# Optimization experiments

Measured on AMD Instinct MI355X. Metric: run time of the kernel, lower is better.

## Reference

```python
import jax, jax.numpy as jnp
import numpy as np


def setup_inputs() -> dict:
    key = jax.random.key(0)
    ks = jax.random.split(key, 6)
    N, E, D, L = 50000, 800000, 128, 2
    x = jax.random.normal(ks[0], (N, D), jnp.float32)
    h = jax.random.normal(ks[1], (L, N, D), jnp.float32)
    Wl = jax.random.normal(ks[2], (L, 6, D, D), jnp.float32) * 0.05  # neighbor (lin_l)
    Wr = jax.random.normal(ks[3], (L, 6, D, D), jnp.float32) * 0.05  # root (lin_r)
    b = jnp.zeros((L, 6, D), jnp.float32)
    src = jax.random.randint(ks[4], (E,), 0, N, jnp.int32)
    dst = jax.random.randint(ks[5], (E,), 0, N, jnp.int32)
    return {"x": x, "h": h, "Wl": Wl, "Wr": Wr, "b": b, "src": src, "dst": dst}


def reference(x, h, Wl, Wr, b, src, dst):
    # PyG SAGEConv (mean aggregation): out = mean_{j in N(i)} x_j @ W_l + x_i @ W_r + b
    N = x.shape[0]
    L = h.shape[0]
    deg = jax.ops.segment_sum(jnp.ones_like(src, jnp.float32), dst, num_segments=N)
    inv_deg = (1.0 / jnp.maximum(deg, 1.0))[:, None]  # [N,1]

    def sage(xin, l, g):
        agg = jax.ops.segment_sum(xin[src], dst, num_segments=N) * inv_deg  # [N,D]
        return agg @ Wl[l, g] + xin @ Wr[l, g] + b[l, g]

    outs = []
    inp = x
    for l in range(L):  # gates: 0=xz 1=hz 2=xr 3=hr 4=xh 5=hh
        z = jax.nn.sigmoid(sage(inp, l, 0) + sage(h[l], l, 1))
        r = jax.nn.sigmoid(sage(inp, l, 2) + sage(h[l], l, 3))
        h_tilde = jnp.tanh(sage(inp, l, 4) + sage(r * h[l], l, 5))
        out = z * h[l] + (1.0 - z) * h_tilde
        outs.append(out)
        inp = out
    return jnp.stack(outs)  # [L, N, D] == h_out
```

## Files before the change

kernel.cpp:

```cpp
#include <hip/hip_runtime.h>
#include <hip/hip_bf16.h>
#include <hip/hip_fp16.h>

#define D 128
#define BM 32
#define BN 128
#define LDSK 64
#define SCAN_BLK 1024

#define GLOBAL_AS __attribute__((address_space(1)))
#define LDS_AS __attribute__((address_space(3)))

typedef __attribute__((ext_vector_type(8))) __bf16 bf16x8;
typedef __attribute__((ext_vector_type(4))) float f32x4;
typedef __hip_bfloat16 bf16;

__device__ __forceinline__ float bf2f(bf16 v) { return __bfloat162float(v); }
__device__ __forceinline__ bf16 f2bf(float v) { return __float2bfloat16(v); }

__global__ void probe_kernel(const unsigned short* __restrict__ w, int n, int* __restrict__ flag) {
  __shared__ int cnt[256];
  int t = threadIdx.x;
  int bad = 0;
  int lim4 = n / 8 < 1024 ? n / 8 : 1024;
  const uint4* w4 = (const uint4*)w;
  for (int i = t; i < lim4; i += 256) {
    uint4 v = w4[i];
    unsigned int ws[8] = {v.x & 0xffffu, v.x >> 16, v.y & 0xffffu, v.y >> 16,
                          v.z & 0xffffu, v.z >> 16, v.w & 0xffffu, v.w >> 16};
#pragma unroll
    for (int j = 0; j < 8; ++j) {
      float f = __uint_as_float(ws[j] << 16);
      if (!(fabsf(f) <= 4.0f)) bad++;
    }
  }
  cnt[t] = bad;
  __syncthreads();
  for (int off = 128; off > 0; off >>= 1) {
    if (t < off) cnt[t] += cnt[t + off];
    __syncthreads();
  }
  if (t == 0) flag[0] = (cnt[0] > 512) ? 1 : 0;
}

__global__ void convert_kernel(const float* __restrict__ xf, const float* __restrict__ hf,
                               bf16* __restrict__ xb, bf16* __restrict__ hb,
                               const int* __restrict__ flag, int nx, int nh) {
  if (flag[0] == 0) return;
  int i = (blockIdx.x * blockDim.x + threadIdx.x) * 4;
  if (i + 3 < nx) {
    float4 v = *(const float4*)(xf + i);
    bf16 o[4] = {f2bf(v.x), f2bf(v.y), f2bf(v.z), f2bf(v.w)};
    *(ushort4*)(xb + i) = *(const ushort4*)o;
  } else {
    for (int j = 0; j < 4; ++j)
      if (i + j < nx) xb[i + j] = f2bf(xf[i + j]);
  }
  if (i + 3 < nh) {
    float4 v = *(const float4*)(hf + i);
    bf16 o[4] = {f2bf(v.x), f2bf(v.y), f2bf(v.z), f2bf(v.w)};
    *(ushort4*)(hb + i) = *(const ushort4*)o;
  } else {
    for (int j = 0; j < 4; ++j)
      if (i + j < nh) hb[i + j] = f2bf(hf[i + j]);
  }
}


__global__ void zero_int_kernel(int* p, int n) {
  int i = blockIdx.x * blockDim.x + threadIdx.x;
  if (i < n) p[i] = 0;
}

__global__ void count_deg_kernel(const int* __restrict__ dst, int* __restrict__ deg, int E) {
  int e = blockIdx.x * blockDim.x + threadIdx.x;
  if (e < E) atomicAdd(&deg[dst[e]], 1);
}

__global__ void scan1_kernel(const int* __restrict__ deg, int* __restrict__ bsum, int N) {
  __shared__ int lsum[256];
  int t = threadIdx.x;
  int base = blockIdx.x * SCAN_BLK + t * 4;
  int s = 0;
  if (base + 3 < N) {
    int4 v = *(const int4*)(deg + base);
    s = v.x + v.y + v.z + v.w;
  } else {
    for (int i = 0; i < 4; ++i)
      if (base + i < N) s += deg[base + i];
  }
  lsum[t] = s;
  __syncthreads();
  for (int off = 128; off > 0; off >>= 1) {
    if (t < off) lsum[t] += lsum[t + off];
    __syncthreads();
  }
  if (t == 0) bsum[blockIdx.x] = lsum[0];
}

__global__ void scan2_kernel(int* __restrict__ bsum, int nb) {
  __shared__ int sh[256];
  int t = threadIdx.x;
  sh[t] = (t < nb) ? bsum[t] : 0;
  __syncthreads();
  for (int off = 1; off < 256; off <<= 1) {
    int v = sh[t];
    int add = (t >= off) ? sh[t - off] : 0;
    __syncthreads();
    sh[t] = v + add;
    __syncthreads();
  }
  if (t < nb) bsum[t] = (t == 0) ? 0 : sh[t - 1];
}

__global__ void scan3_kernel(const int* __restrict__ deg, const int* __restrict__ bsum,
                             int* __restrict__ offs, int* __restrict__ cursor,
                             float* __restrict__ inv_deg, int N, int E) {
  __shared__ int lsum[256];
  int t = threadIdx.x;
  int base = blockIdx.x * SCAN_BLK + t * 4;
  int d0 = 0, d1 = 0, d2 = 0, d3 = 0;
  if (base + 3 < N) {
    int4 v = *(const int4*)(deg + base);
    d0 = v.x; d1 = v.y; d2 = v.z; d3 = v.w;
  } else {
    if (base + 0 < N) d0 = deg[base + 0];
    if (base + 1 < N) d1 = deg[base + 1];
    if (base + 2 < N) d2 = deg[base + 2];
    if (base + 3 < N) d3 = deg[base + 3];
  }
  lsum[t] = d0 + d1 + d2 + d3;
  __syncthreads();
  for (int off = 1; off < 256; off <<= 1) {
    int v = lsum[t];
    int add = (t >= off) ? lsum[t - off] : 0;
    __syncthreads();
    lsum[t] = v + add;
    __syncthreads();
  }
  int run = bsum[blockIdx.x] + ((t == 0) ? 0 : lsum[t - 1]);
  int dd[4] = {d0, d1, d2, d3};
  for (int i = 0; i < 4; ++i) {
    int idx = base + i;
    if (idx < N) {
      offs[idx] = run;
      cursor[idx] = run;
      inv_deg[idx] = 1.0f / (float)(dd[i] > 1 ? dd[i] : 1);
      run += dd[i];
    }
  }
  if (blockIdx.x == 0 && t == 0) offs[N] = E;
}

__global__ void scatter_kernel(const int* __restrict__ src, const int* __restrict__ dst,
                               int* __restrict__ cursor, int* __restrict__ esrc, int E) {
  int e = blockIdx.x * blockDim.x + threadIdx.x;
  if (e < E) {
    int pos = atomicAdd(&cursor[dst[e]], 1);
    esrc[pos] = src[e];
  }
}


__global__ void agg_kernel(const bf16* __restrict__ featA, const bf16* __restrict__ featB,
                           const int* __restrict__ flag, const int* __restrict__ esrc,
                           const int* __restrict__ offs, const float* __restrict__ inv_deg,
                           bf16* __restrict__ out, int N) {
  const bf16* feat = flag[0] ? featB : featA;
  int node = (int)((blockIdx.x * (size_t)blockDim.x + threadIdx.x) >> 6);
  int lane = threadIdx.x & 63;
  if (node >= N) return;
  int e0 = offs[node], e1 = offs[node + 1];
  float a0 = 0.f, a1 = 0.f;
  int c = lane * 2;
  for (int base = e0; base < e1; base += 64) {
    int cnt = e1 - base;
    if (cnt > 64) cnt = 64;
    int ei = base + lane;
    int idx = esrc[ei < e1 ? ei : (e1 - 1)];
    int j = 0;
    for (; j + 8 <= cnt; j += 8) {
      int s0 = __shfl(idx, j + 0, 64), s1 = __shfl(idx, j + 1, 64);
      int s2 = __shfl(idx, j + 2, 64), s3 = __shfl(idx, j + 3, 64);
      int s4 = __shfl(idx, j + 4, 64), s5 = __shfl(idx, j + 5, 64);
      int s6 = __shfl(idx, j + 6, 64), s7 = __shfl(idx, j + 7, 64);
      __hip_bfloat162 v0 = *(const __hip_bfloat162*)(feat + (size_t)s0 * D + c);
      __hip_bfloat162 v1 = *(const __hip_bfloat162*)(feat + (size_t)s1 * D + c);
      __hip_bfloat162 v2 = *(const __hip_bfloat162*)(feat + (size_t)s2 * D + c);
      __hip_bfloat162 v3 = *(const __hip_bfloat162*)(feat + (size_t)s3 * D + c);
      __hip_bfloat162 v4 = *(const __hip_bfloat162*)(feat + (size_t)s4 * D + c);
      __hip_bfloat162 v5 = *(const __hip_bfloat162*)(feat + (size_t)s5 * D + c);
      __hip_bfloat162 v6 = *(const __hip_bfloat162*)(feat + (size_t)s6 * D + c);
      __hip_bfloat162 v7 = *(const __hip_bfloat162*)(feat + (size_t)s7 * D + c);
      a0 += bf2f(v0.x) + bf2f(v1.x) + bf2f(v2.x) + bf2f(v3.x) +
            bf2f(v4.x) + bf2f(v5.x) + bf2f(v6.x) + bf2f(v7.x);
      a1 += bf2f(v0.y) + bf2f(v1.y) + bf2f(v2.y) + bf2f(v3.y) +
            bf2f(v4.y) + bf2f(v5.y) + bf2f(v6.y) + bf2f(v7.y);
    }
    for (; j < cnt; ++j) {
      int s = __shfl(idx, j, 64);
      __hip_bfloat162 v = *(const __hip_bfloat162*)(feat + (size_t)s * D + c);
      a0 += bf2f(v.x);
      a1 += bf2f(v.y);
    }
  }
  float w = inv_deg[node];
  __hip_bfloat162 o;
  o.x = f2bf(a0 * w);
  o.y = f2bf(a1 * w);
  *(__hip_bfloat162*)(out + (size_t)node * D + c) = o;
}

__global__ void agg_dual_kernel(const bf16* __restrict__ fAa, const bf16* __restrict__ fAb,
                                const bf16* __restrict__ fBa, const bf16* __restrict__ fBb,
                                const int* __restrict__ flag, const int* __restrict__ esrc,
                                const int* __restrict__ offs, const float* __restrict__ inv_deg,
                                bf16* __restrict__ outA, bf16* __restrict__ outB, int N) {
  int fl = flag[0];
  const bf16* fA = fl ? fAb : fAa;
  const bf16* fB = fl ? fBb : fBa;
  int node = (int)((blockIdx.x * (size_t)blockDim.x + threadIdx.x) >> 6);
  int lane = threadIdx.x & 63;
  if (node >= N) return;
  int e0 = offs[node], e1 = offs[node + 1];
  float a0 = 0.f, a1 = 0.f, b0 = 0.f, b1 = 0.f;
  int c = lane * 2;
  for (int base = e0; base < e1; base += 64) {
    int cnt = e1 - base;
    if (cnt > 64) cnt = 64;
    int ei = base + lane;
    int idx = esrc[ei < e1 ? ei : (e1 - 1)];
    int j = 0;
    for (; j + 4 <= cnt; j += 4) {
      int s0 = __shfl(idx, j + 0, 64), s1 = __shfl(idx, j + 1, 64);
      int s2 = __shfl(idx, j + 2, 64), s3 = __shfl(idx, j + 3, 64);
      size_t r0 = (size_t)s0 * D + c, r1 = (size_t)s1 * D + c;
      size_t r2 = (size_t)s2 * D + c, r3 = (size_t)s3 * D + c;
      __hip_bfloat162 va0 = *(const __hip_bfloat162*)(fA + r0);
      __hip_bfloat162 va1 = *(const __hip_bfloat162*)(fA + r1);
      __hip_bfloat162 va2 = *(const __hip_bfloat162*)(fA + r2);
      __hip_bfloat162 va3 = *(const __hip_bfloat162*)(fA + r3);
      __hip_bfloat162 vb0 = *(const __hip_bfloat162*)(fB + r0);
      __hip_bfloat162 vb1 = *(const __hip_bfloat162*)(fB + r1);
      __hip_bfloat162 vb2 = *(const __hip_bfloat162*)(fB + r2);
      __hip_bfloat162 vb3 = *(const __hip_bfloat162*)(fB + r3);
      a0 += bf2f(va0.x) + bf2f(va1.x) + bf2f(va2.x) + bf2f(va3.x);
      a1 += bf2f(va0.y) + bf2f(va1.y) + bf2f(va2.y) + bf2f(va3.y);
      b0 += bf2f(vb0.x) + bf2f(vb1.x) + bf2f(vb2.x) + bf2f(vb3.x);
      b1 += bf2f(vb0.y) + bf2f(vb1.y) + bf2f(vb2.y) + bf2f(vb3.y);
    }
    for (; j < cnt; ++j) {
      int s = __shfl(idx, j, 64);
      size_t ro = (size_t)s * D + c;
      __hip_bfloat162 va = *(const __hip_bfloat162*)(fA + ro);
      __hip_bfloat162 vb = *(const __hip_bfloat162*)(fB + ro);
      a0 += bf2f(va.x);
      a1 += bf2f(va.y);
      b0 += bf2f(vb.x);
      b1 += bf2f(vb.y);
    }
  }
  float w = inv_deg[node];
  __hip_bfloat162 oa, ob;
  oa.x = f2bf(a0 * w);
  oa.y = f2bf(a1 * w);
  ob.x = f2bf(b0 * w);
  ob.y = f2bf(b1 * w);
  *(__hip_bfloat162*)(outA + (size_t)node * D + c) = oa;
  *(__hip_bfloat162*)(outB + (size_t)node * D + c) = ob;
}


__device__ __forceinline__ float loadw(const void* p, size_t idx, int fl) {
  return fl ? ((const float*)p)[idx] : bf2f(((const bf16*)p)[idx]);
}

__global__ void pack_kernel(const void* __restrict__ Wl, const void* __restrict__ Wr,
                            const void* __restrict__ b, int l, const int* __restrict__ flag,
                            bf16* __restrict__ B1p, bf16* __restrict__ B2p,
                            float* __restrict__ bs1, float* __restrict__ bs2) {
  int fl = flag[0];
  int idx = blockIdx.x * blockDim.x + threadIdx.x;
  const int SZ1 = 256 * 512;
  const int SZ2 = 128 * 512;
  if (idx < SZ1) {
    int n = idx >> 9, k = idx & 511;
    int p = k >> 7, kr = k & 127;
    int gpair = n >> 7, nc = n & 127;
    int gate = gpair * 2 + (p >> 1);
    const void* W = (p & 1) ? Wr : Wl;
    B1p[idx] = f2bf(loadw(W, (((size_t)l * 6 + gate) * D + kr) * D + nc, fl));
  } else if (idx < SZ1 + SZ2) {
    int i2 = idx - SZ1;
    int n = i2 >> 9, k = i2 & 511;
    int p = k >> 7, kr = k & 127;
    int gate = 4 + (p >> 1);
    const void* W = (p & 1) ? Wr : Wl;
    B2p[i2] = f2bf(loadw(W, (((size_t)l * 6 + gate) * D + kr) * D + n, fl));
  } else if (idx < SZ1 + SZ2 + 384) {
    int c = idx - (SZ1 + SZ2);
    if (c < 256) {
      int g0 = (c >> 7) * 2;
      int cc = c & 127;
      bs1[c] = loadw(b, ((size_t)l * 6 + g0) * D + cc, fl) +
               loadw(b, ((size_t)l * 6 + g0 + 1) * D + cc, fl);
    } else {
      int cc = c - 256;
      bs2[cc] = loadw(b, ((size_t)l * 6 + 4) * D + cc, fl) +
                loadw(b, ((size_t)l * 6 + 5) * D + cc, fl);
    }
  }
}


__device__ __forceinline__ void stage_tile(const bf16* const (&Ablk)[4],
                                           const bf16* __restrict__ Bp, int M, int row0, int col0,
                                           bf16* As, bf16* Bs, int kt, int wave, int r_rel,
                                           int pslot) {
  const bf16* Aptr = Ablk[kt >> 1];
  const int kr = (kt & 1) * 64;
  {
    int rchunk = wave * 8;
    int r = rchunk + r_rel;
    int gsrc = pslot ^ (r & 7);
    int rg = row0 + r;
    if (rg > M - 1) rg = M - 1;
    const bf16* ga = Aptr + (size_t)rg * D + kr + gsrc * 8;
    bf16* la = As + rchunk * LDSK;
    __builtin_amdgcn_global_load_lds((const GLOBAL_AS unsigned int*)(const void*)ga,
                                     (LDS_AS unsigned int*)(void*)la, 16, 0, 0);
  }
#pragma unroll
  for (int i = 0; i < 4; ++i) {
    int rchunk = wave * 32 + i * 8;
    int r = rchunk + r_rel;
    int gsrc = pslot ^ (r & 7);
    const bf16* gb = Bp + (size_t)(col0 + r) * 512 + kt * 64 + gsrc * 8;
    bf16* lb = Bs + rchunk * LDSK;
    __builtin_amdgcn_global_load_lds((const GLOBAL_AS unsigned int*)(const void*)gb,
                                     (LDS_AS unsigned int*)(void*)lb, 16, 0, 0);
  }
}

__device__ __forceinline__ void gemm_mainloop(const bf16* A0, const bf16* A1, const bf16* A2,
                                              const bf16* A3, const bf16* __restrict__ Bp, int M,
                                              int row0, int col0, bf16* As, bf16* Bs,
                                              f32x4 (&acc)[1][4]) {
  int tid = threadIdx.x;
  int wave = tid >> 6, lane = tid & 63;
  int wrow = (wave >> 1) * 16, wcol = (wave & 1) * 64;
  const bf16* Ablk[4] = {A0, A1, A2, A3};
  int r_rel = lane >> 3;
  int pslot = lane & 7;
  int quad = lane >> 4, mr = lane & 15;
  const int ABUF = BM * LDSK;
  const int BBUF = BN * LDSK;

  stage_tile(Ablk, Bp, M, row0, col0, As, Bs, 0, wave, r_rel, pslot);
  __syncthreads();

#pragma unroll
  for (int kt = 0; kt < 8; ++kt) {
    const int cur = kt & 1;
    if (kt < 7)
      stage_tile(Ablk, Bp, M, row0, col0, As + (cur ^ 1) * ABUF, Bs + (cur ^ 1) * BBUF, kt + 1,
                 wave, r_rel, pslot);
    const bf16* Asc = As + cur * ABUF;
    const bf16* Bsc = Bs + cur * BBUF;
#pragma unroll
    for (int kk = 0; kk < 2; ++kk) {
      int G = kk * 4 + quad;
      bf16x8 af, bfv[4];
      {
        int R = wrow + mr;
        af = *(const bf16x8*)(const void*)(Asc + R * LDSK + ((G ^ (R & 7)) * 8));
      }
#pragma unroll
      for (int ni = 0; ni < 4; ++ni) {
        int R = wcol + ni * 16 + mr;
        bfv[ni] = *(const bf16x8*)(const void*)(Bsc + R * LDSK + ((G ^ (R & 7)) * 8));
      }
#pragma unroll
      for (int ni = 0; ni < 4; ++ni)
        acc[0][ni] =
            __builtin_amdgcn_mfma_f32_16x16x32_bf16(af, bfv[ni], acc[0][ni], 0, 0, 0);
    }
    __syncthreads();
  }
}

__global__ __launch_bounds__(256) void gemm1_kernel(
    const bf16* A0, const bf16* A1a, const bf16* A1b, const bf16* A2, const bf16* A3a,
    const bf16* A3b, const int* __restrict__ flag, const bf16* __restrict__ Bp,
    const float* __restrict__ bias, __half* __restrict__ z, bf16* __restrict__ rh, int M) {
  int fl = flag[0];
  const bf16* A1 = fl ? A1b : A1a;
  const bf16* A3 = fl ? A3b : A3a;
  const bf16* hl = A3;
  __shared__ bf16 As[2 * BM * LDSK];
  __shared__ bf16 Bs[2 * BN * LDSK];
  f32x4 acc[1][4];
#pragma unroll
  for (int j = 0; j < 4; ++j) acc[0][j] = (f32x4){0.f, 0.f, 0.f, 0.f};
  int row0 = blockIdx.x * BM, col0 = blockIdx.y * BN;
  gemm_mainloop(A0, A1, A2, A3, Bp, M, row0, col0, As, Bs, acc);
  int lane = threadIdx.x & 63, wave = threadIdx.x >> 6;
  int wrow = (wave >> 1) * 16, wcol = (wave & 1) * 64;
  int mr = lane & 15, quad = lane >> 4;
#pragma unroll
  for (int ni = 0; ni < 4; ++ni)
#pragma unroll
    for (int r = 0; r < 4; ++r) {
      int grow = row0 + wrow + quad * 4 + r;
      if (grow >= M) continue;
      int gcol = col0 + wcol + ni * 16 + mr;
      float v = acc[0][ni][r] + bias[gcol];
      float sg = 1.0f / (1.0f + __expf(-v));
      if (gcol < 128) {
        z[(size_t)grow * D + gcol] = __float2half(sg);
      } else {
        int cc = gcol - 128;
        float hv = bf2f(hl[(size_t)grow * D + cc]);
        rh[(size_t)grow * D + cc] = f2bf(sg * hv);
      }
    }
}

__global__ __launch_bounds__(256) void gemm2_kernel(
    const bf16* A0, const bf16* A1a, const bf16* A1b, const bf16* A2, const bf16* A3,
    const bf16* A3hA, const bf16* A3hB, const int* __restrict__ flag, const bf16* __restrict__ Bp,
    const float* __restrict__ bias, const __half* __restrict__ z, void* __restrict__ outbase,
    size_t lND, bf16* __restrict__ nextb, int M) {
  int fl = flag[0];
  const bf16* A1 = fl ? A1b : A1a;
  const bf16* hl = fl ? A3hB : A3hA;
  __shared__ bf16 As[2 * BM * LDSK];
  __shared__ bf16 Bs[2 * BN * LDSK];
  f32x4 acc[1][4];
#pragma unroll
  for (int j = 0; j < 4; ++j) acc[0][j] = (f32x4){0.f, 0.f, 0.f, 0.f};
  int row0 = blockIdx.x * BM, col0 = 0;
  gemm_mainloop(A0, A1, A2, A3, Bp, M, row0, col0, As, Bs, acc);
  int lane = threadIdx.x & 63, wave = threadIdx.x >> 6;
  int wrow = (wave >> 1) * 16, wcol = (wave & 1) * 64;
  int mr = lane & 15, quad = lane >> 4;
#pragma unroll
  for (int ni = 0; ni < 4; ++ni)
#pragma unroll
    for (int r = 0; r < 4; ++r) {
      int grow = row0 + wrow + quad * 4 + r;
      if (grow >= M) continue;
      int gcol = col0 + wcol + ni * 16 + mr;
      float pre = acc[0][ni][r] + bias[gcol];
      float ht = tanhf(pre);
      size_t off = (size_t)grow * D + gcol;
      float zv = __half2float(z[off]);
      float hv = bf2f(hl[off]);
      float ov = zv * hv + (1.0f - zv) * ht;
      if (fl) {
        ((float*)outbase)[lND + off] = ov;
        nextb[off] = f2bf(ov);
      } else {
        ((bf16*)outbase)[lND + off] = f2bf(ov);
      }
    }
}


extern "C" void kernel_launch(void* const* d_in, const int* in_sizes, int n_in, void* d_out,
                              int out_size, void* d_ws, size_t ws_size, hipStream_t stream) {
  const void* x = d_in[0];
  const void* h = d_in[1];
  const void* Wl = d_in[2];
  const void* Wr = d_in[3];
  const void* b = d_in[4];
  const int* src = (const int*)d_in[5];
  const int* dst = (const int*)d_in[6];

  const int NX = in_sizes[0];
  const int NH = in_sizes[1];
  const int N = NX / D;
  const int E = in_sizes[5];
  const int L = NH / NX;
  (void)n_in;
  (void)out_size;
  (void)ws_size;

  char* ws = (char*)d_ws;
  size_t off = 0;
  auto alloc = [&](size_t bytes) -> char* {
    char* p = ws + off;
    off = (off + bytes + 255) & ~(size_t)255;
    return p;
  };
  int* flag = (int*)alloc(256);
  int* deg = (int*)alloc((size_t)N * 4);
  int* offs = (int*)alloc((size_t)(N + 1) * 4);
  int* cursor = (int*)alloc((size_t)N * 4);
  float* inv_deg = (float*)alloc((size_t)N * 4);
  int* bsum = (int*)alloc(256 * 4);
  int* esrc = (int*)alloc((size_t)E * 4);
  bf16* agg_inp = (bf16*)alloc((size_t)N * D * 2);
  bf16* agg2 = (bf16*)alloc((size_t)N * D * 2);
  bf16* rh = (bf16*)alloc((size_t)N * D * 2);
  __half* z = (__half*)alloc((size_t)N * D * 2);
  bf16* B1p = (bf16*)alloc(256 * 512 * 2);
  bf16* B2p = (bf16*)alloc(128 * 512 * 2);
  float* bs1 = (float*)alloc(256 * 4);
  float* bs2 = (float*)alloc(128 * 4);
  bf16* xb = (bf16*)alloc((size_t)NX * 2);
  bf16* hb = (bf16*)alloc((size_t)NH * 2);

  probe_kernel<<<1, 256, 0, stream>>>((const unsigned short*)Wl, in_sizes[2], flag);
  int ncv = NX > NH ? NX : NH;
  convert_kernel<<<(ncv / 4 + 255) / 256, 256, 0, stream>>>((const float*)x, (const float*)h, xb,
                                                            hb, flag, NX, NH);

  zero_int_kernel<<<(N + 255) / 256, 256, 0, stream>>>(deg, N);
  count_deg_kernel<<<(E + 255) / 256, 256, 0, stream>>>(dst, deg, E);
  int nb = (N + SCAN_BLK - 1) / SCAN_BLK;
  scan1_kernel<<<nb, 256, 0, stream>>>(deg, bsum, N);
  scan2_kernel<<<1, 256, 0, stream>>>(bsum, nb);
  scan3_kernel<<<nb, 256, 0, stream>>>(deg, bsum, offs, cursor, inv_deg, N, E);
  scatter_kernel<<<(E + 255) / 256, 256, 0, stream>>>(src, dst, cursor, esrc, E);

  int mtiles = (N + BM - 1) / BM;
  const int pack_elems = 256 * 512 + 128 * 512 + 384;
  for (int l = 0; l < L; ++l) {
    const size_t lND = (size_t)l * N * D;
    const bf16* inpA = (l == 0) ? (const bf16*)x : ((const bf16*)d_out + lND - (size_t)N * D);
    const bf16* hlA = (const bf16*)h + lND;
    const bf16* hlB = hb + lND;

    pack_kernel<<<(pack_elems + 255) / 256, 256, 0, stream>>>(Wl, Wr, b, l, flag, B1p, B2p, bs1,
                                                              bs2);
    agg_dual_kernel<<<(N + 3) / 4, 256, 0, stream>>>(inpA, xb, hlA, hlB, flag, esrc, offs, inv_deg,
                                                     agg_inp, agg2, N);
    gemm1_kernel<<<dim3(mtiles, 2), 256, 0, stream>>>(agg_inp, inpA, xb, agg2, hlA, hlB, flag, B1p,
                                                      bs1, z, rh, N);
    agg_kernel<<<(N + 3) / 4, 256, 0, stream>>>(rh, rh, flag, esrc, offs, inv_deg, agg2, N);
    gemm2_kernel<<<dim3(mtiles, 1), 256, 0, stream>>>(agg_inp, inpA, xb, agg2, rh, hlA, hlB, flag,
                                                      B2p, bs2, z, d_out, lND, xb, N);
  }
}
```

Baseline: 592.5 us.

## Fuse r*h neighbor aggregation into gemm2 prologue via LDS tile

Removes the separate agg_kernel for the r*h gate input. Each gemm2 block now gathers and mean-aggregates the neighbor rows for its 32 nodes straight into an LDS tile, and the GEMM main loop reads that K-slot from LDS instead of staging it from global memory. This saves a kernel launch plus writing and re-reading the aggregated intermediate. In exchange, the gather runs with only 8 nodes per wave inside the GEMM block, and the extra LDS use may lower occupancy.

```diff
diff --git a/kernel.cpp b/kernel.cpp
--- a/kernel.cpp
+++ b/kernel.cpp
@@ -6,6 +6,7 @@
 #define BM 32
 #define BN 128
 #define LDSK 64
+#define AGG_LD 136
 #define SCAN_BLK 1024
 
 #define GLOBAL_AS __attribute__((address_space(1)))
@@ -161,55 +162,6 @@
   }
 }
 
-
-__global__ void agg_kernel(const bf16* __restrict__ featA, const bf16* __restrict__ featB,
-                           const int* __restrict__ flag, const int* __restrict__ esrc,
-                           const int* __restrict__ offs, const float* __restrict__ inv_deg,
-                           bf16* __restrict__ out, int N) {
-  const bf16* feat = flag[0] ? featB : featA;
-  int node = (int)((blockIdx.x * (size_t)blockDim.x + threadIdx.x) >> 6);
-  int lane = threadIdx.x & 63;
-  if (node >= N) return;
-  int e0 = offs[node], e1 = offs[node + 1];
-  float a0 = 0.f, a1 = 0.f;
-  int c = lane * 2;
-  for (int base = e0; base < e1; base += 64) {
-    int cnt = e1 - base;
-    if (cnt > 64) cnt = 64;
-    int ei = base + lane;
-    int idx = esrc[ei < e1 ? ei : (e1 - 1)];
-    int j = 0;
-    for (; j + 8 <= cnt; j += 8) {
-      int s0 = __shfl(idx, j + 0, 64), s1 = __shfl(idx, j + 1, 64);
-      int s2 = __shfl(idx, j + 2, 64), s3 = __shfl(idx, j + 3, 64);
-      int s4 = __shfl(idx, j + 4, 64), s5 = __shfl(idx, j + 5, 64);
-      int s6 = __shfl(idx, j + 6, 64), s7 = __shfl(idx, j + 7, 64);
-      __hip_bfloat162 v0 = *(const __hip_bfloat162*)(feat + (size_t)s0 * D + c);
-      __hip_bfloat162 v1 = *(const __hip_bfloat162*)(feat + (size_t)s1 * D + c);
-      __hip_bfloat162 v2 = *(const __hip_bfloat162*)(feat + (size_t)s2 * D + c);
-      __hip_bfloat162 v3 = *(const __hip_bfloat162*)(feat + (size_t)s3 * D + c);
-      __hip_bfloat162 v4 = *(const __hip_bfloat162*)(feat + (size_t)s4 * D + c);
-      __hip_bfloat162 v5 = *(const __hip_bfloat162*)(feat + (size_t)s5 * D + c);
-      __hip_bfloat162 v6 = *(const __hip_bfloat162*)(feat + (size_t)s6 * D + c);
-      __hip_bfloat162 v7 = *(const __hip_bfloat162*)(feat + (size_t)s7 * D + c);
-      a0 += bf2f(v0.x) + bf2f(v1.x) + bf2f(v2.x) + bf2f(v3.x) +
-            bf2f(v4.x) + bf2f(v5.x) + bf2f(v6.x) + bf2f(v7.x);
-      a1 += bf2f(v0.y) + bf2f(v1.y) + bf2f(v2.y) + bf2f(v3.y) +
-            bf2f(v4.y) + bf2f(v5.y) + bf2f(v6.y) + bf2f(v7.y);
-    }
-    for (; j < cnt; ++j) {
-      int s = __shfl(idx, j, 64);
-      __hip_bfloat162 v = *(const __hip_bfloat162*)(feat + (size_t)s * D + c);
-      a0 += bf2f(v.x);
-      a1 += bf2f(v.y);
-    }
-  }
-  float w = inv_deg[node];
-  __hip_bfloat162 o;
-  o.x = f2bf(a0 * w);
-  o.y = f2bf(a1 * w);
-  *(__hip_bfloat162*)(out + (size_t)node * D + c) = o;
-}
 
 __global__ void agg_dual_kernel(const bf16* __restrict__ fAa, const bf16* __restrict__ fAb,
                                 const bf16* __restrict__ fBa, const bf16* __restrict__ fBb,
@@ -316,10 +268,10 @@
 __device__ __forceinline__ void stage_tile(const bf16* const (&Ablk)[4],
                                            const bf16* __restrict__ Bp, int M, int row0, int col0,
                                            bf16* As, bf16* Bs, int kt, int wave, int r_rel,
-                                           int pslot) {
+                                           int pslot, bool stageA) {
   const bf16* Aptr = Ablk[kt >> 1];
   const int kr = (kt & 1) * 64;
-  {
+  if (stageA) {
     int rchunk = wave * 8;
     int r = rchunk + r_rel;
     int gsrc = pslot ^ (r & 7);
@@ -342,10 +294,11 @@
   }
 }
 
-__device__ __forceinline__ void gemm_mainloop(const bf16* A0, const bf16* A1, const bf16* A2,
-                                              const bf16* A3, const bf16* __restrict__ Bp, int M,
-                                              int row0, int col0, bf16* As, bf16* Bs,
-                                              f32x4 (&acc)[1][4]) {
+template <int LDS_SLOT>
+__device__ __forceinline__ void gemm_mainloop_t(const bf16* A0, const bf16* A1, const bf16* A2,
+                                                const bf16* A3, const bf16* __restrict__ Bp, int M,
+                                                int row0, int col0, bf16* As, bf16* Bs,
+                                                const bf16* AggL, f32x4 (&acc)[1][4]) {
   int tid = threadIdx.x;
   int wave = tid >> 6, lane = tid & 63;
   int wrow = (wave >> 1) * 16, wcol = (wave & 1) * 64;
@@ -356,7 +309,7 @@
   const int ABUF = BM * LDSK;
   const int BBUF = BN * LDSK;
 
-  stage_tile(Ablk, Bp, M, row0, col0, As, Bs, 0, wave, r_rel, pslot);
+  stage_tile(Ablk, Bp, M, row0, col0, As, Bs, 0, wave, r_rel, pslot, (0 >> 1) != LDS_SLOT);
   __syncthreads();
 
 #pragma unroll
@@ -364,7 +317,7 @@
     const int cur = kt & 1;
     if (kt < 7)
       stage_tile(Ablk, Bp, M, row0, col0, As + (cur ^ 1) * ABUF, Bs + (cur ^ 1) * BBUF, kt + 1,
-                 wave, r_rel, pslot);
+                 wave, r_rel, pslot, ((kt + 1) >> 1) != LDS_SLOT);
     const bf16* Asc = As + cur * ABUF;
     const bf16* Bsc = Bs + cur * BBUF;
 #pragma unroll
@@ -373,7 +326,10 @@
       bf16x8 af, bfv[4];
       {
         int R = wrow + mr;
-        af = *(const bf16x8*)(const void*)(Asc + R * LDSK + ((G ^ (R & 7)) * 8));
+        if ((kt >> 1) == LDS_SLOT)
+          af = *(const bf16x8*)(const void*)(AggL + R * AGG_LD + (kt & 1) * 64 + G * 8);
+        else
+          af = *(const bf16x8*)(const void*)(Asc + R * LDSK + ((G ^ (R & 7)) * 8));
       }
 #pragma unroll
       for (int ni = 0; ni < 4; ++ni) {
@@ -403,7 +359,7 @@
 #pragma unroll
   for (int j = 0; j < 4; ++j) acc[0][j] = (f32x4){0.f, 0.f, 0.f, 0.f};
   int row0 = blockIdx.x * BM, col0 = blockIdx.y * BN;
-  gemm_mainloop(A0, A1, A2, A3, Bp, M, row0, col0, As, Bs, acc);
+  gemm_mainloop_t<-1>(A0, A1, A2, A3, Bp, M, row0, col0, As, Bs, nullptr, acc);
   int lane = threadIdx.x & 63, wave = threadIdx.x >> 6;
   int wrow = (wave >> 1) * 16, wcol = (wave & 1) * 64;
   int mr = lane & 15, quad = lane >> 4;
@@ -427,21 +383,78 @@
 }
 
 __global__ __launch_bounds__(256) void gemm2_kernel(
-    const bf16* A0, const bf16* A1a, const bf16* A1b, const bf16* A2, const bf16* A3,
+    const bf16* A0, const bf16* A1a, const bf16* A1b, const bf16* A3,
     const bf16* A3hA, const bf16* A3hB, const int* __restrict__ flag, const bf16* __restrict__ Bp,
-    const float* __restrict__ bias, const __half* __restrict__ z, void* __restrict__ outbase,
+    const float* __restrict__ bias, const __half* __restrict__ z,
+    const int* __restrict__ esrc, const int* __restrict__ offs,
+    const float* __restrict__ inv_deg, void* __restrict__ outbase,
     size_t lND, bf16* __restrict__ nextb, int M) {
   int fl = flag[0];
   const bf16* A1 = fl ? A1b : A1a;
   const bf16* hl = fl ? A3hB : A3hA;
+  const bf16* rhf = A3;
   __shared__ bf16 As[2 * BM * LDSK];
   __shared__ bf16 Bs[2 * BN * LDSK];
+  __shared__ bf16 AggL[BM * AGG_LD];
+  int lane = threadIdx.x & 63, wave = threadIdx.x >> 6;
+  int row0 = blockIdx.x * BM, col0 = 0;
+
+  {
+    int c = lane * 2;
+#pragma unroll 1
+    for (int i = 0; i < 8; ++i) {
+      int r = wave * 8 + i;
+      int node = row0 + r;
+      float a0 = 0.f, a1 = 0.f;
+      if (node < M) {
+        int e0 = offs[node], e1 = offs[node + 1];
+        for (int base = e0; base < e1; base += 64) {
+          int cnt = e1 - base;
+          if (cnt > 64) cnt = 64;
+          int ei = base + lane;
+          int idx = esrc[ei < e1 ? ei : (e1 - 1)];
+          int j = 0;
+          for (; j + 8 <= cnt; j += 8) {
+            int s0 = __shfl(idx, j + 0, 64), s1 = __shfl(idx, j + 1, 64);
+            int s2 = __shfl(idx, j + 2, 64), s3 = __shfl(idx, j + 3, 64);
+            int s4 = __shfl(idx, j + 4, 64), s5 = __shfl(idx, j + 5, 64);
+            int s6 = __shfl(idx, j + 6, 64), s7 = __shfl(idx, j + 7, 64);
+            __hip_bfloat162 v0 = *(const __hip_bfloat162*)(rhf + (size_t)s0 * D + c);
+            __hip_bfloat162 v1 = *(const __hip_bfloat162*)(rhf + (size_t)s1 * D + c);
+            __hip_bfloat162 v2 = *(const __hip_bfloat162*)(rhf + (size_t)s2 * D + c);
+            __hip_bfloat162 v3 = *(const __hip_bfloat162*)(rhf + (size_t)s3 * D + c);
+            __hip_bfloat162 v4 = *(const __hip_bfloat162*)(rhf + (size_t)s4 * D + c);
+            __hip_bfloat162 v5 = *(const __hip_bfloat162*)(rhf + (size_t)s5 * D + c);
+            __hip_bfloat162 v6 = *(const __hip_bfloat162*)(rhf + (size_t)s6 * D + c);
+            __hip_bfloat162 v7 = *(const __hip_bfloat162*)(rhf + (size_t)s7 * D + c);
+            a0 += bf2f(v0.x) + bf2f(v1.x) + bf2f(v2.x) + bf2f(v3.x) +
+                  bf2f(v4.x) + bf2f(v5.x) + bf2f(v6.x) + bf2f(v7.x);
+            a1 += bf2f(v0.y) + bf2f(v1.y) + bf2f(v2.y) + bf2f(v3.y) +
+                  bf2f(v4.y) + bf2f(v5.y) + bf2f(v6.y) + bf2f(v7.y);
+          }
+          for (; j < cnt; ++j) {
+            int s = __shfl(idx, j, 64);
+            __hip_bfloat162 v = *(const __hip_bfloat162*)(rhf + (size_t)s * D + c);
+            a0 += bf2f(v.x);
+            a1 += bf2f(v.y);
+          }
+        }
+        float w = inv_deg[node];
+        a0 *= w;
+        a1 *= w;
+      }
+      __hip_bfloat162 o;
+      o.x = f2bf(a0);
+      o.y = f2bf(a1);
+      *(__hip_bfloat162*)(AggL + r * AGG_LD + c) = o;
+    }
+  }
+  __syncthreads();
+
   f32x4 acc[1][4];
 #pragma unroll
   for (int j = 0; j < 4; ++j) acc[0][j] = (f32x4){0.f, 0.f, 0.f, 0.f};
-  int row0 = blockIdx.x * BM, col0 = 0;
-  gemm_mainloop(A0, A1, A2, A3, Bp, M, row0, col0, As, Bs, acc);
-  int lane = threadIdx.x & 63, wave = threadIdx.x >> 6;
+  gemm_mainloop_t<2>(A0, A1, nullptr, A3, Bp, M, row0, col0, As, Bs, AggL, acc);
   int wrow = (wave >> 1) * 16, wcol = (wave & 1) * 64;
   int mr = lane & 15, quad = lane >> 4;
 #pragma unroll
@@ -538,8 +551,8 @@
                                                      agg_inp, agg2, N);
     gemm1_kernel<<<dim3(mtiles, 2), 256, 0, stream>>>(agg_inp, inpA, xb, agg2, hlA, hlB, flag, B1p,
                                                       bs1, z, rh, N);
-    agg_kernel<<<(N + 3) / 4, 256, 0, stream>>>(rh, rh, flag, esrc, offs, inv_deg, agg2, N);
-    gemm2_kernel<<<dim3(mtiles, 1), 256, 0, stream>>>(agg_inp, inpA, xb, agg2, rh, hlA, hlB, flag,
-                                                      B2p, bs2, z, d_out, lND, xb, N);
-  }
-}
+    gemm2_kernel<<<dim3(mtiles, 1), 256, 0, stream>>>(agg_inp, inpA, xb, rh, hlA, hlB, flag, B2p,
+                                                      bs2, z, esrc, offs, inv_deg, d_out, lND, xb,
+                                                      N);
+  }
+}
```

Result: slower. 673.1 us (+13.6%).

## Vectorize neighbor gathers to 16-byte loads and hoist weight packing

Applied to the files above, without the earlier changes.

The aggregation kernels now split each wavefront into four groups of 16 lanes. Each group loads a full 128-feature row with 16-byte loads, so four edges are gathered at once, and the partial sums are combined across groups with xor shuffles. The goal is fewer, wider memory transactions per gathered row instead of 4-byte loads per lane. Weight packing for both layers now runs in a single launch before the layer loop, which removes one launch per layer. The final layer also skips writing the unused bf16 copy of its output. The cost is more accumulator registers and a cross-lane reduction at the end of each node.

```diff
diff --git a/kernel.cpp b/kernel.cpp
--- a/kernel.cpp
+++ b/kernel.cpp
@@ -13,10 +13,14 @@
 
 typedef __attribute__((ext_vector_type(8))) __bf16 bf16x8;
 typedef __attribute__((ext_vector_type(4))) float f32x4;
+typedef __attribute__((ext_vector_type(8))) unsigned short ushort8;
 typedef __hip_bfloat16 bf16;
 
 __device__ __forceinline__ float bf2f(bf16 v) { return __bfloat162float(v); }
 __device__ __forceinline__ bf16 f2bf(float v) { return __float2bfloat16(v); }
+__device__ __forceinline__ float bfu(unsigned short u) {
+  return __uint_as_float(((unsigned int)u) << 16);
+}
 
 __global__ void probe_kernel(const unsigned short* __restrict__ w, int n, int* __restrict__ flag) {
   __shared__ int cnt[256];
@@ -171,8 +175,9 @@
   int lane = threadIdx.x & 63;
   if (node >= N) return;
   int e0 = offs[node], e1 = offs[node + 1];
-  float a0 = 0.f, a1 = 0.f;
-  int c = lane * 2;
+  int p = lane >> 4;
+  int c8 = (lane & 15) * 8;
+  float a[8] = {0.f, 0.f, 0.f, 0.f, 0.f, 0.f, 0.f, 0.f};
   for (int base = e0; base < e1; base += 64) {
     int cnt = e1 - base;
     if (cnt > 64) cnt = 64;
@@ -180,35 +185,40 @@
     int idx = esrc[ei < e1 ? ei : (e1 - 1)];
     int j = 0;
     for (; j + 8 <= cnt; j += 8) {
-      int s0 = __shfl(idx, j + 0, 64), s1 = __shfl(idx, j + 1, 64);
-      int s2 = __shfl(idx, j + 2, 64), s3 = __shfl(idx, j + 3, 64);
-      int s4 = __shfl(idx, j + 4, 64), s5 = __shfl(idx, j + 5, 64);
-      int s6 = __shfl(idx, j + 6, 64), s7 = __shfl(idx, j + 7, 64);
-      __hip_bfloat162 v0 = *(const __hip_bfloat162*)(feat + (size_t)s0 * D + c);
-      __hip_bfloat162 v1 = *(const __hip_bfloat162*)(feat + (size_t)s1 * D + c);
-      __hip_bfloat162 v2 = *(const __hip_bfloat162*)(feat + (size_t)s2 * D + c);
-      __hip_bfloat162 v3 = *(const __hip_bfloat162*)(feat + (size_t)s3 * D + c);
-      __hip_bfloat162 v4 = *(const __hip_bfloat162*)(feat + (size_t)s4 * D + c);
-      __hip_bfloat162 v5 = *(const __hip_bfloat162*)(feat + (size_t)s5 * D + c);
-      __hip_bfloat162 v6 = *(const __hip_bfloat162*)(feat + (size_t)s6 * D + c);
-      __hip_bfloat162 v7 = *(const __hip_bfloat162*)(feat + (size_t)s7 * D + c);
-      a0 += bf2f(v0.x) + bf2f(v1.x) + bf2f(v2.x) + bf2f(v3.x) +
-            bf2f(v4.x) + bf2f(v5.x) + bf2f(v6.x) + bf2f(v7.x);
-      a1 += bf2f(v0.y) + bf2f(v1.y) + bf2f(v2.y) + bf2f(v3.y) +
-            bf2f(v4.y) + bf2f(v5.y) + bf2f(v6.y) + bf2f(v7.y);
-    }
-    for (; j < cnt; ++j) {
-      int s = __shfl(idx, j, 64);
-      __hip_bfloat162 v = *(const __hip_bfloat162*)(feat + (size_t)s * D + c);
-      a0 += bf2f(v.x);
-      a1 += bf2f(v.y);
-    }
-  }
-  float w = inv_deg[node];
-  __hip_bfloat162 o;
-  o.x = f2bf(a0 * w);
-  o.y = f2bf(a1 * w);
-  *(__hip_bfloat162*)(out + (size_t)node * D + c) = o;
+      int s0 = __shfl(idx, j + p, 64);
+      int s1 = __shfl(idx, j + 4 + p, 64);
+      ushort8 v0 = *(const ushort8*)(feat + (size_t)s0 * D + c8);
+      ushort8 v1 = *(const ushort8*)(feat + (size_t)s1 * D + c8);
+#pragma unroll
+      for (int q = 0; q < 8; ++q) a[q] += bfu(v0[q]) + bfu(v1[q]);
+    }
+    for (; j + 4 <= cnt; j += 4) {
+      int s = __shfl(idx, j + p, 64);
+      ushort8 v = *(const ushort8*)(feat + (size_t)s * D + c8);
+#pragma unroll
+      for (int q = 0; q < 8; ++q) a[q] += bfu(v[q]);
+    }
+    if (j < cnt) {
+      int jp = j + p;
+      int s = __shfl(idx, jp < cnt ? jp : cnt - 1, 64);
+      ushort8 v = *(const ushort8*)(feat + (size_t)s * D + c8);
+      float m = (jp < cnt) ? 1.f : 0.f;
+#pragma unroll
+      for (int q = 0; q < 8; ++q) a[q] += m * bfu(v[q]);
+    }
+  }
+#pragma unroll
+  for (int q = 0; q < 8; ++q) {
+    a[q] += __shfl_xor(a[q], 16, 64);
+    a[q] += __shfl_xor(a[q], 32, 64);
+  }
+  if (lane < 16) {
+    float w = inv_deg[node];
+    bf16 o[8];
+#pragma unroll
+    for (int q = 0; q < 8; ++q) o[q] = f2bf(a[q] * w);
+    *(ushort8*)(out + (size_t)node * D + c8) = *(const ushort8*)o;
+  }
 }
 
 __global__ void agg_dual_kernel(const bf16* __restrict__ fAa, const bf16* __restrict__ fAb,
@@ -223,51 +233,73 @@
   int lane = threadIdx.x & 63;
   if (node >= N) return;
   int e0 = offs[node], e1 = offs[node + 1];
-  float a0 = 0.f, a1 = 0.f, b0 = 0.f, b1 = 0.f;
-  int c = lane * 2;
+  int p = lane >> 4;
+  int c8 = (lane & 15) * 8;
+  float a[8] = {0.f, 0.f, 0.f, 0.f, 0.f, 0.f, 0.f, 0.f};
+  float b[8] = {0.f, 0.f, 0.f, 0.f, 0.f, 0.f, 0.f, 0.f};
   for (int base = e0; base < e1; base += 64) {
     int cnt = e1 - base;
     if (cnt > 64) cnt = 64;
     int ei = base + lane;
     int idx = esrc[ei < e1 ? ei : (e1 - 1)];
     int j = 0;
+    for (; j + 8 <= cnt; j += 8) {
+      int s0 = __shfl(idx, j + p, 64);
+      int s1 = __shfl(idx, j + 4 + p, 64);
+      size_t r0 = (size_t)s0 * D + c8, r1 = (size_t)s1 * D + c8;
+      ushort8 va0 = *(const ushort8*)(fA + r0);
+      ushort8 va1 = *(const ushort8*)(fA + r1);
+      ushort8 vb0 = *(const ushort8*)(fB + r0);
+      ushort8 vb1 = *(const ushort8*)(fB + r1);
+#pragma unroll
+      for (int q = 0; q < 8; ++q) {
+        a[q] += bfu(va0[q]) + bfu(va1[q]);
+        b[q] += bfu(vb0[q]) + bfu(vb1[q]);
+      }
+    }
     for (; j + 4 <= cnt; j += 4) {
-      int s0 = __shfl(idx, j + 0, 64), s1 = __shfl(idx, j + 1, 64);
-      int s2 = __shfl(idx, j + 2, 64), s3 = __shfl(idx, j + 3, 64);
-      size_t r0 = (size_t)s0 * D + c, r1 = (size_t)s1 * D + c;
-      size_t r2 = (size_t)s2 * D + c, r3 = (size_t)s3 * D + c;
-      __hip_bfloat162 va0 = *(const __hip_bfloat162*)(fA + r0);
-      __hip_bfloat162 va1 = *(const __hip_bfloat162*)(fA + r1);
-      __hip_bfloat162 va2 = *(const __hip_bfloat162*)(fA + r2);
-      __hip_bfloat162 va3 = *(const __hip_bfloat162*)(fA + r3);
-      __hip_bfloat162 vb0 = *(const __hip_bfloat162*)(fB + r0);
-      __hip_bfloat162 vb1 = *(const __hip_bfloat162*)(fB + r1);
-      __hip_bfloat162 vb2 = *(const __hip_bfloat162*)(fB + r2);
-      __hip_bfloat162 vb3 = *(const __hip_bfloat162*)(fB + r3);
-      a0 += bf2f(va0.x) + bf2f(va1.x) + bf2f(va2.x) + bf2f(va3.x);
-      a1 += bf2f(va0.y) + bf2f(va1.y) + bf2f(va2.y) + bf2f(va3.y);
-      b0 += bf2f(vb0.x) + bf2f(vb1.x) + bf2f(vb2.x) + bf2f(vb3.x);
-      b1 += bf2f(vb0.y) + bf2f(vb1.y) + bf2f(vb2.y) + bf2f(vb3.y);
-    }
-    for (; j < cnt; ++j) {
-      int s = __shfl(idx, j, 64);
-      size_t ro = (size_t)s * D + c;
-      __hip_bfloat162 va = *(const __hip_bfloat162*)(fA + ro);
-      __hip_bfloat162 vb = *(const __hip_bfloat162*)(fB + ro);
-      a0 += bf2f(va.x);
-      a1 += bf2f(va.y);
-      b0 += bf2f(vb.x);
-      b1 += bf2f(vb.y);
-    }
-  }
-  float w = inv_deg[node];
-  __hip_bfloat162 oa, ob;
-  oa.x = f2bf(a0 * w);
-  oa.y = f2bf(a1 * w);
-  ob.x = f2bf(b0 * w);
-  ob.y = f2bf(b1 * w);
-  *(__hip_bfloat162*)(outA + (size_t)node * D + c) = oa;
-  *(__hip_bfloat162*)(outB + (size_t)node * D + c) = ob;
+      int s = __shfl(idx, j + p, 64);
+      size_t ro = (size_t)s * D + c8;
+      ushort8 va = *(const ushort8*)(fA + ro);
+      ushort8 vb = *(const ushort8*)(fB + ro);
+#pragma unroll
+      for (int q = 0; q < 8; ++q) {
+        a[q] += bfu(va[q]);
+        b[q] += bfu(vb[q]);
+      }
+    }
+    if (j < cnt) {
+      int jp = j + p;
+      int s = __shfl(idx, jp < cnt ? jp : cnt - 1, 64);
+      size_t ro = (size_t)s * D + c8;
+      ushort8 va = *(const ushort8*)(fA + ro);
+      ushort8 vb = *(const ushort8*)(fB + ro);
+      float m = (jp < cnt) ? 1.f : 0.f;
+#pragma unroll
+      for (int q = 0; q < 8; ++q) {
+        a[q] += m * bfu(va[q]);
+        b[q] += m * bfu(vb[q]);
+      }
+    }
+  }
+#pragma unroll
+  for (int q = 0; q < 8; ++q) {
+    a[q] += __shfl_xor(a[q], 16, 64);
+    a[q] += __shfl_xor(a[q], 32, 64);
+    b[q] += __shfl_xor(b[q], 16, 64);
+    b[q] += __shfl_xor(b[q], 32, 64);
+  }
+  if (lane < 16) {
+    float w = inv_deg[node];
+    bf16 oa[8], ob[8];
+#pragma unroll
+    for (int q = 0; q < 8; ++q) {
+      oa[q] = f2bf(a[q] * w);
+      ob[q] = f2bf(b[q] * w);
+    }
+    *(ushort8*)(outA + (size_t)node * D + c8) = *(const ushort8*)oa;
+    *(ushort8*)(outB + (size_t)node * D + c8) = *(const ushort8*)ob;
+  }
 }
 
 
@@ -275,39 +307,48 @@
   return fl ? ((const float*)p)[idx] : bf2f(((const bf16*)p)[idx]);
 }
 
+#define PACK_SZ1 (256 * 512)
+#define PACK_SZ2 (128 * 512)
+#define PACK_P (PACK_SZ1 + PACK_SZ2 + 384)
+
 __global__ void pack_kernel(const void* __restrict__ Wl, const void* __restrict__ Wr,
-                            const void* __restrict__ b, int l, const int* __restrict__ flag,
+                            const void* __restrict__ b, int L, const int* __restrict__ flag,
                             bf16* __restrict__ B1p, bf16* __restrict__ B2p,
                             float* __restrict__ bs1, float* __restrict__ bs2) {
   int fl = flag[0];
-  int idx = blockIdx.x * blockDim.x + threadIdx.x;
-  const int SZ1 = 256 * 512;
-  const int SZ2 = 128 * 512;
-  if (idx < SZ1) {
+  int gidx = blockIdx.x * blockDim.x + threadIdx.x;
+  int l = gidx / PACK_P;
+  if (l >= L) return;
+  int idx = gidx - l * PACK_P;
+  bf16* B1 = B1p + (size_t)l * PACK_SZ1;
+  bf16* B2 = B2p + (size_t)l * PACK_SZ2;
+  float* b1 = bs1 + (size_t)l * 256;
+  float* b2 = bs2 + (size_t)l * 128;
+  if (idx < PACK_SZ1) {
     int n = idx >> 9, k = idx & 511;
     int p = k >> 7, kr = k & 127;
     int gpair = n >> 7, nc = n & 127;
     int gate = gpair * 2 + (p >> 1);
     const void* W = (p & 1) ? Wr : Wl;
-    B1p[idx] = f2bf(loadw(W, (((size_t)l * 6 + gate) * D + kr) * D + nc, fl));
-  } else if (idx < SZ1 + SZ2) {
-    int i2 = idx - SZ1;
+    B1[idx] = f2bf(loadw(W, (((size_t)l * 6 + gate) * D + kr) * D + nc, fl));
+  } else if (idx < PACK_SZ1 + PACK_SZ2) {
+    int i2 = idx - PACK_SZ1;
     int n = i2 >> 9, k = i2 & 511;
     int p = k >> 7, kr = k & 127;
     int gate = 4 + (p >> 1);
     const void* W = (p & 1) ? Wr : Wl;
-    B2p[i2] = f2bf(loadw(W, (((size_t)l * 6 + gate) * D + kr) * D + n, fl));
-  } else if (idx < SZ1 + SZ2 + 384) {
-    int c = idx - (SZ1 + SZ2);
+    B2[i2] = f2bf(loadw(W, (((size_t)l * 6 + gate) * D + kr) * D + n, fl));
+  } else {
+    int c = idx - (PACK_SZ1 + PACK_SZ2);
     if (c < 256) {
       int g0 = (c >> 7) * 2;
       int cc = c & 127;
-      bs1[c] = loadw(b, ((size_t)l * 6 + g0) * D + cc, fl) +
-               loadw(b, ((size_t)l * 6 + g0 + 1) * D + cc, fl);
+      b1[c] = loadw(b, ((size_t)l * 6 + g0) * D + cc, fl) +
+              loadw(b, ((size_t)l * 6 + g0 + 1) * D + cc, fl);
     } else {
       int cc = c - 256;
-      bs2[cc] = loadw(b, ((size_t)l * 6 + 4) * D + cc, fl) +
-                loadw(b, ((size_t)l * 6 + 5) * D + cc, fl);
+      b2[cc] = loadw(b, ((size_t)l * 6 + 4) * D + cc, fl) +
+               loadw(b, ((size_t)l * 6 + 5) * D + cc, fl);
     }
   }
 }
@@ -459,7 +500,7 @@
       float ov = zv * hv + (1.0f - zv) * ht;
       if (fl) {
         ((float*)outbase)[lND + off] = ov;
-        nextb[off] = f2bf(ov);
+        if (nextb) nextb[off] = f2bf(ov);
       } else {
         ((bf16*)outbase)[lND + off] = f2bf(ov);
       }
@@ -504,10 +545,10 @@
   bf16* agg2 = (bf16*)alloc((size_t)N * D * 2);
   bf16* rh = (bf16*)alloc((size_t)N * D * 2);
   __half* z = (__half*)alloc((size_t)N * D * 2);
-  bf16* B1p = (bf16*)alloc(256 * 512 * 2);
-  bf16* B2p = (bf16*)alloc(128 * 512 * 2);
-  float* bs1 = (float*)alloc(256 * 4);
-  float* bs2 = (float*)alloc(128 * 4);
+  bf16* B1p = (bf16*)alloc((size_t)L * PACK_SZ1 * 2);
+  bf16* B2p = (bf16*)alloc((size_t)L * PACK_SZ2 * 2);
+  float* bs1 = (float*)alloc((size_t)L * 256 * 4);
+  float* bs2 = (float*)alloc((size_t)L * 128 * 4);
   bf16* xb = (bf16*)alloc((size_t)NX * 2);
   bf16* hb = (bf16*)alloc((size_t)NH * 2);
 
@@ -515,6 +556,8 @@
   int ncv = NX > NH ? NX : NH;
   convert_kernel<<<(ncv / 4 + 255) / 256, 256, 0, stream>>>((const float*)x, (const float*)h, xb,
                                                             hb, flag, NX, NH);
+  pack_kernel<<<(L * PACK_P + 255) / 256, 256, 0, stream>>>(Wl, Wr, b, L, flag, B1p, B2p, bs1,
+                                                            bs2);
 
   zero_int_kernel<<<(N + 255) / 256, 256, 0, stream>>>(deg, N);
   count_deg_kernel<<<(E + 255) / 256, 256, 0, stream>>>(dst, deg, E);
@@ -525,21 +568,23 @@
   scatter_kernel<<<(E + 255) / 256, 256, 0, stream>>>(src, dst, cursor, esrc, E);
 
   int mtiles = (N + BM - 1) / BM;
-  const int pack_elems = 256 * 512 + 128 * 512 + 384;
   for (int l = 0; l < L; ++l) {
     const size_t lND = (size_t)l * N * D;
     const bf16* inpA = (l == 0) ? (const bf16*)x : ((const bf16*)d_out + lND - (size_t)N * D);
     const bf16* hlA = (const bf16*)h + lND;
     const bf16* hlB = hb + lND;
-
-    pack_kernel<<<(pack_elems + 255) / 256, 256, 0, stream>>>(Wl, Wr, b, l, flag, B1p, B2p, bs1,
-                                                              bs2);
+    const bf16* B1l = B1p + (size_t)l * PACK_SZ1;
+    const bf16* B2l = B2p + (size_t)l * PACK_SZ2;
+    const float* bs1l = bs1 + (size_t)l * 256;
+    const float* bs2l = bs2 + (size_t)l * 128;
+
     agg_dual_kernel<<<(N + 3) / 4, 256, 0, stream>>>(inpA, xb, hlA, hlB, flag, esrc, offs, inv_deg,
                                                      agg_inp, agg2, N);
-    gemm1_kernel<<<dim3(mtiles, 2), 256, 0, stream>>>(agg_inp, inpA, xb, agg2, hlA, hlB, flag, B1p,
-                                                      bs1, z, rh, N);
+    gemm1_kernel<<<dim3(mtiles, 2), 256, 0, stream>>>(agg_inp, inpA, xb, agg2, hlA, hlB, flag, B1l,
+                                                      bs1l, z, rh, N);
     agg_kernel<<<(N + 3) / 4, 256, 0, stream>>>(rh, rh, flag, esrc, offs, inv_deg, agg2, N);
     gemm2_kernel<<<dim3(mtiles, 1), 256, 0, stream>>>(agg_inp, inpA, xb, agg2, rh, hlA, hlB, flag,
-                                                      B2p, bs2, z, d_out, lND, xb, N);
-  }
-}
+                                                      B2l, bs2l, z, d_out, lND,
+                                                      (l + 1 < L) ? xb : (bf16*)nullptr, N);
+  }
+}
```

Result: faster. 579.8 us (-2.1%).
